# Kernel tuning notes

Measured on AMD Instinct MI355X. Metric: run time of the kernel, lower is better.

## Reference

```python
import jax, jax.numpy as jnp
import numpy as np

B, S, K = 128, 196, 512   # batch, encoder seq, keys_hidden_size
T_CAP = 16                # caption length (out_seq_len = 15)
V, E, H = 32000, 512, 512 # vocab, embedding, hidden


def setup_inputs() -> dict:
    key = jax.random.key(0)
    ks = jax.random.split(key, 16)
    sc = lambda fan_in: 1.0 / np.sqrt(fan_in)
    return {
        "features": jax.random.normal(ks[0], (B, S, K), jnp.float32),
        "captions": jax.random.randint(ks[1], (B, T_CAP), 0, V),
        "emb": jax.random.normal(ks[2], (V, E), jnp.float32) * 0.02,
        "fc1_w": jax.random.normal(ks[3], (H, E), jnp.float32) * sc(E),
        "fc1_b": jnp.zeros((H,), jnp.float32),
        "att_wq": jax.random.normal(ks[4], (H, H), jnp.float32) * sc(H),
        "att_wk": jax.random.normal(ks[5], (H, K), jnp.float32) * sc(K),
        "att_v": jax.random.normal(ks[6], (H,), jnp.float32) * sc(H),
        "fc0_w": jax.random.normal(ks[7], (H, K), jnp.float32) * sc(K),
        "fc0_b": jnp.zeros((H,), jnp.float32),
        "gru_wih": jax.random.normal(ks[8], (3 * H, 2 * H), jnp.float32) * sc(2 * H),
        "gru_whh": jax.random.normal(ks[9], (3 * H, H), jnp.float32) * sc(H),
        "gru_bih": jnp.zeros((3 * H,), jnp.float32),
        "gru_bhh": jnp.zeros((3 * H,), jnp.float32),
        "fc2_w": jax.random.normal(ks[10], (V, H), jnp.float32) * sc(H),
        "fc2_b": jnp.zeros((V,), jnp.float32),
    }


def reference(features, captions, emb, fc1_w, fc1_b, att_wq, att_wk, att_v,
              fc0_w, fc0_b, gru_wih, gru_whh, gru_bih, gru_bhh, fc2_w, fc2_b):
    # embed captions and project: (B, T_CAP, H)
    x = emb[captions] @ fc1_w.T + fc1_b
    # precompute key projection for Bahdanau attention: (B, S, H)
    keys_proj = features @ att_wk.T

    def step(h, x_t):
        # Bahdanau additive attention
        q = h @ att_wq.T                                   # (B, H)
        scores = jnp.tanh(q[:, None, :] + keys_proj) @ att_v  # (B, S)
        w = jax.nn.softmax(scores, axis=1)
        context = jnp.einsum('bs,bsk->bk', w, features)    # (B, K)
        context = context @ fc0_w.T + fc0_b                # fc_0 -> (B, H)
        rnn_in = jnp.concatenate([x_t, context], axis=-1)  # (B, 2H)
        # GRU cell, torch gate order (r, z, n)
        gi = rnn_in @ gru_wih.T + gru_bih
        gh = h @ gru_whh.T + gru_bhh
        ir, iz, inn = jnp.split(gi, 3, axis=-1)
        hr, hz, hn = jnp.split(gh, 3, axis=-1)
        r = jax.nn.sigmoid(ir + hr)
        z = jax.nn.sigmoid(iz + hz)
        n = jnp.tanh(inn + r * hn)
        h_new = (1.0 - z) * n + z * h
        out = h_new @ fc2_w.T + fc2_b                      # fc_2 -> (B, V)
        return h_new, out

    out_seq_len = captions.shape[1] - 1
    xs = jnp.swapaxes(x[:, :out_seq_len], 0, 1)            # (T, B, H)
    h0 = jnp.zeros((features.shape[0], fc0_b.shape[0]), features.dtype)
    _, outs = jax.lax.scan(step, h0, xs)                   # (T, B, V)
    return jnp.swapaxes(outs, 0, 1)                        # (B, T, V)
```

## Files before the change

### kernel.cpp

```cpp
#include <hip/hip_runtime.h>

typedef _Float16 half_t;
typedef float    floatx4 __attribute__((ext_vector_type(4)));
typedef _Float16 halfx8  __attribute__((ext_vector_type(8)));
typedef _Float16 halfx2  __attribute__((ext_vector_type(2)));

__device__ __forceinline__ float tanh_f(float x) {
  float e = __expf(2.0f * x);
  return 1.0f - 2.0f / (e + 1.0f);
}
__device__ __forceinline__ float sigmoid_f(float x) {
  return 1.0f / (1.0f + __expf(-x));
}

__device__ __forceinline__ void gl16(const void* g, void* s) {
  __builtin_amdgcn_global_load_lds((__attribute__((address_space(1))) unsigned int*)g,
                                   (__attribute__((address_space(3))) unsigned int*)s,
                                   16, 0, 0);
}

__device__ __forceinline__ int xcd_swz(int bid, int nwg) {
  int q = nwg >> 3, r = nwg & 7, x = bid & 7, p = bid >> 3;
  return (x < r ? x * (q + 1) : r * (q + 1) + (x - r) * q) + p;
}

__device__ __forceinline__ void cvt4(const float* __restrict__ src,
                                     half_t* __restrict__ dst, int blk) {
  int i = (blk * 256 + threadIdx.x) * 4;
  float4 v = *(const float4*)(src + i);
  halfx2 a; a[0] = (half_t)v.x; a[1] = (half_t)v.y;
  halfx2 b; b[0] = (half_t)v.z; b[1] = (half_t)v.w;
  *(halfx2*)(dst + i) = a;
  *(halfx2*)(dst + i + 2) = b;
}

__global__ __launch_bounds__(256) void k_prep(const float* __restrict__ fc2_w, half_t* __restrict__ fc2w_h,
                                              const float* __restrict__ features, half_t* __restrict__ featf,
                                              const float* __restrict__ fc1_w, half_t* __restrict__ fc1w_h,
                                              const float* __restrict__ att_wk, const float* __restrict__ fc0_w,
                                              half_t* __restrict__ wkfc0,
                                              const float* __restrict__ gru_whh, const float* __restrict__ att_wq,
                                              half_t* __restrict__ bcat2,
                                              const float* __restrict__ gru_wih, half_t* __restrict__ wihx,
                                              half_t* __restrict__ wihc,
                                              const float* __restrict__ emb, const int* __restrict__ cap,
                                              half_t* __restrict__ embg,
                                              const float* __restrict__ fc0_b, float* __restrict__ biasc,
                                              float4* __restrict__ zbase) {
  const int bb = blockIdx.x, tid = threadIdx.x;
  if (bb < 16000) {
    cvt4(fc2_w, fc2w_h, bb);
  } else if (bb < 28544) {
    cvt4(features, featf, bb - 16000);
  } else if (bb < 28800) {
    cvt4(fc1_w, fc1w_h, bb - 28544);
  } else if (bb < 29056) {
    cvt4(att_wk, wkfc0, bb - 28800);
  } else if (bb < 29312) {
    cvt4(fc0_w, wkfc0 + (size_t)512 * 512, bb - 29056);
  } else if (bb < 30080) {
    cvt4(gru_whh, bcat2, bb - 29312);
  } else if (bb < 30336) {
    cvt4(att_wq, bcat2 + (size_t)1536 * 512, bb - 30080);
  } else if (bb < 31872) {
    int row = bb - 30336, j = tid * 2;
    float2 a = *(const float2*)(gru_wih + (size_t)row * 1024 + j);
    float2 b = *(const float2*)(gru_wih + (size_t)row * 1024 + 512 + j);
    halfx2 ax; ax[0] = (half_t)a.x; ax[1] = (half_t)a.y;
    halfx2 bx; bx[0] = (half_t)b.x; bx[1] = (half_t)b.y;
    *(halfx2*)(wihx + (size_t)row * 512 + j) = ax;
    *(halfx2*)(wihc + (size_t)row * 512 + j) = bx;
  } else if (bb < 33792) {
    int row = bb - 31872;
    int b = row / 15, t = row - b * 15;
    int c = cap[b * 16 + t];
    const float* s = emb + (size_t)c * 512;
    int e = tid * 2;
    float2 v = *(const float2*)(s + e);
    halfx2 o; o[0] = (half_t)v.x; o[1] = (half_t)v.y;
    *(halfx2*)(embg + (size_t)row * 512 + e) = o;
  } else if (bb < 33796) {
    int i = (bb - 33792) * 256 + tid;
    biasc[i] = (i < 512) ? 0.f : fc0_b[i - 512];
  } else {
    zbase[(size_t)(bb - 33796) * 256 + tid] = make_float4(0.f, 0.f, 0.f, 0.f);
  }
}

__device__ __forceinline__ void gemm128_mfma(const half_t* __restrict__ Ap,
                                             const half_t* __restrict__ Bp,
                                             const int Kd,
                                             const int m0, const int n0,
                                             char* smem, floatx4 (&acc)[4][4]) {
  constexpr int ABYTES = 128 * 32 * 2;
  constexpr int BBYTES = 128 * 32 * 2;

  const int l = threadIdx.x & 63;
  const int w = threadIdx.x >> 6;

  const half_t* gA = Ap + (size_t)(m0 + w * 32 + (l >> 2)) * Kd + (l & 3) * 8;
  const half_t* gB = Bp + (size_t)(n0 + w * 32 + (l >> 2)) * Kd + (l & 3) * 8;

  const int fr = l & 15;
  const int kq = (l >> 4) * 8;
  const int mh = (w & 1) * 64;
  const int nh = (w >> 1) * 64;

#pragma unroll
  for (int i = 0; i < 4; ++i)
#pragma unroll
    for (int j = 0; j < 4; ++j) { floatx4 z = {0.f, 0.f, 0.f, 0.f}; acc[i][j] = z; }

  const int NT = Kd >> 5;

  auto stage = [&](int tt) {
    const int k0 = tt * 32;
    char* aD = smem + (tt & 1) * ABYTES;
    char* bD = smem + 2 * ABYTES + (tt & 1) * BBYTES;
    const half_t* g = gA + k0;
    gl16(g, aD + (w * 32) * 64);
    gl16(g + (size_t)16 * Kd, aD + (w * 32 + 16) * 64);
    const half_t* g2 = gB + k0;
    gl16(g2, bD + (w * 32) * 64);
    gl16(g2 + (size_t)16 * Kd, bD + (w * 32 + 16) * 64);
  };

  stage(0);

  for (int t = 0; t < NT; ++t) {
    __syncthreads();
    if (t + 1 < NT) stage(t + 1);
    const char* aB = smem + (t & 1) * ABYTES;
    const char* bB = smem + 2 * ABYTES + (t & 1) * BBYTES;
    halfx8 af[4], bf[4];
#pragma unroll
    for (int i = 0; i < 4; ++i) {
      af[i] = *(const halfx8*)((const half_t*)aB + (size_t)(mh + i * 16 + fr) * 32 + kq);
      bf[i] = *(const halfx8*)((const half_t*)bB + (size_t)(nh + i * 16 + fr) * 32 + kq);
    }
#pragma unroll
    for (int i = 0; i < 4; ++i)
#pragma unroll
      for (int j = 0; j < 4; ++j)
        acc[i][j] = __builtin_amdgcn_mfma_f32_16x16x32_f16(af[i], bf[j], acc[i][j], 0, 0, 0);
  }
}

template <bool OUT_F16>
__device__ __forceinline__ void gemm128_body(const half_t* __restrict__ Ap,
                                             const half_t* __restrict__ Bp,
                                             const float* __restrict__ bias,
                                             void* __restrict__ Cp,
                                             const int Kd, const int ldc,
                                             const int m0, const int n0,
                                             char* smem) {
  const int l = threadIdx.x & 63;
  const int w = threadIdx.x >> 6;
  const int mh = (w & 1) * 64;
  const int nh = (w >> 1) * 64;
  floatx4 acc[4][4];
  gemm128_mfma(Ap, Bp, Kd, m0, n0, smem, acc);

#pragma unroll
  for (int j = 0; j < 4; ++j) {
    const int n = n0 + nh + j * 16 + (l & 15);
    const float bv = bias ? bias[n] : 0.0f;
#pragma unroll
    for (int i = 0; i < 4; ++i) {
      const int mb = m0 + mh + i * 16 + (l >> 4) * 4;
#pragma unroll
      for (int r = 0; r < 4; ++r) {
        const float v = acc[i][j][r] + bv;
        const size_t ci = (size_t)(mb + r) * ldc + n;
        if constexpr (OUT_F16) ((half_t*)Cp)[ci] = (half_t)v;
        else                   ((float*)Cp)[ci] = v;
      }
    }
  }
}

template <bool OUT_F16>
__global__ __launch_bounds__(256) void k_gemm_lds(const half_t* __restrict__ Ap,
                                                  const half_t* __restrict__ Bp,
                                                  const float* __restrict__ bias,
                                                  void* __restrict__ Cp,
                                                  int Kd, int ldc) {
  __shared__ __align__(16) char smem[32768];
  gemm128_body<OUT_F16>(Ap, Bp, bias, Cp, Kd, ldc,
                        blockIdx.y * 128, blockIdx.x * 128, smem);
}

__global__ __launch_bounds__(256) void k_kpfp(const half_t* __restrict__ featf,
                                              const half_t* __restrict__ wkfc0,
                                              const float* __restrict__ biasc,
                                              half_t* __restrict__ kpfp) {
  __shared__ __align__(16) char smem[32768];
  const int w = (blockIdx.x & 7) * 196 + (blockIdx.x >> 3);
  const int n0 = (w & 7) * 128;
  const int m0 = (w >> 3) * 128;
  gemm128_body<true>(featf, wkfc0, biasc, kpfp, 512, 1024, m0, n0, smem);
}

__global__ __launch_bounds__(256) void k_fc2_final(const half_t* __restrict__ hall,
                                                   const half_t* __restrict__ fc2w,
                                                   const float* __restrict__ fc2b,
                                                   float* __restrict__ outp) {
  __shared__ __align__(16) char smem[64 * 132 * 4];
  const int wk = xcd_swz(blockIdx.x, 3750);
  const int m0 = (wk % 15) * 128;
  const int n0 = (wk / 15) * 128;

  const int tid = threadIdx.x;
  const int l = tid & 63;
  const int w = tid >> 6;
  const int nh = (w >> 1) * 64;

  floatx4 acc[4][4];
  gemm128_mfma(hall, fc2w, 512, m0, n0, smem, acc);

  const float4 bv4 = *(const float4*)(fc2b + n0 + (tid & 31) * 4);
  float* sf = (float*)smem;

#pragma unroll
  for (int h = 0; h < 2; ++h) {
    __syncthreads();
    if ((w & 1) == h) {
#pragma unroll
      for (int i = 0; i < 4; ++i)
#pragma unroll
        for (int j = 0; j < 4; ++j)
#pragma unroll
          for (int r = 0; r < 4; ++r)
            sf[(i * 16 + (l >> 4) * 4 + r) * 132 + nh + j * 16 + (l & 15)] = acc[i][j][r];
    }
    __syncthreads();
#pragma unroll
    for (int it = 0; it < 8; ++it) {
      const int row = it * 8 + (tid >> 5);
      float4 v = *(const float4*)&sf[row * 132 + (tid & 31) * 4];
      v.x += bv4.x; v.y += bv4.y; v.z += bv4.z; v.w += bv4.w;
      *(float4*)(outp + (size_t)(m0 + h * 64 + row) * 32000 + n0 + (tid & 31) * 4) = v;
    }
  }
}

__global__ __launch_bounds__(256) void k_scores(const half_t* __restrict__ kpfp,
                                                const float* __restrict__ ghq,
                                                const float* __restrict__ attv,
                                                float* __restrict__ scores) {
  int w = blockIdx.x * 4 + (threadIdx.x >> 6);
  int l = threadIdx.x & 63;
  int b = w / 196;
  halfx8 kv = *(const halfx8*)(kpfp + (size_t)w * 1024 + l * 8);
  const float* qr = ghq + (size_t)b * 2048 + 1536 + l * 8;
  float4 q0 = *(const float4*)qr;
  float4 q1 = *(const float4*)(qr + 4);
  float4 a0 = *(const float4*)(attv + l * 8);
  float4 a1 = *(const float4*)(attv + l * 8 + 4);
  float acc = a0.x * tanh_f(q0.x + (float)kv[0]);
  acc += a0.y * tanh_f(q0.y + (float)kv[1]);
  acc += a0.z * tanh_f(q0.z + (float)kv[2]);
  acc += a0.w * tanh_f(q0.w + (float)kv[3]);
  acc += a1.x * tanh_f(q1.x + (float)kv[4]);
  acc += a1.y * tanh_f(q1.y + (float)kv[5]);
  acc += a1.z * tanh_f(q1.z + (float)kv[6]);
  acc += a1.w * tanh_f(q1.w + (float)kv[7]);
#pragma unroll
  for (int off = 32; off > 0; off >>= 1) acc += __shfl_xor(acc, off, 64);
  if (l == 0) scores[w] = acc;
}

__global__ __launch_bounds__(256) void k_ctx(const float* __restrict__ scores,
                                             const half_t* __restrict__ kpfp,
                                             half_t* __restrict__ ctxo) {
  const int b = blockIdx.x, kt = blockIdx.y * 128, t = threadIdx.x;
  __shared__ float sw[196], red[256];
  float sc = (t < 196) ? scores[b * 196 + t] : -1e30f;
  red[t] = sc; __syncthreads();
  for (int o = 128; o > 0; o >>= 1) { if (t < o) red[t] = fmaxf(red[t], red[t + o]); __syncthreads(); }
  float mx = red[0]; __syncthreads();
  float e = (t < 196) ? __expf(sc - mx) : 0.f;
  red[t] = e; __syncthreads();
  for (int o = 128; o > 0; o >>= 1) { if (t < o) red[t] += red[t + o]; __syncthreads(); }
  float inv = 1.0f / red[0];
  if (t < 196) sw[t] = e * inv;
  __syncthreads();
  const int kk = t & 127, half = t >> 7, s0 = half * 98;
  const half_t* fp = kpfp + (size_t)(b * 196 + s0) * 1024 + 512 + kt + kk;
  float acc = 0.f;
#pragma unroll 7
  for (int i = 0; i < 98; ++i) acc += sw[s0 + i] * (float)fp[(size_t)i * 1024];
  red[t] = acc; __syncthreads();
  if (t < 128) ctxo[(size_t)b * 512 + kt + t] = (half_t)(red[t] + red[t + 128]);
}

__global__ __launch_bounds__(256) void k_gates(const float* __restrict__ gix,
                                               const float* __restrict__ gic,
                                               const float* __restrict__ ghq,
                                               const float* __restrict__ bih,
                                               const float* __restrict__ bhh,
                                               float* __restrict__ hbuf,
                                               half_t* __restrict__ hh,
                                               half_t* __restrict__ hall, int step) {
  int idx = blockIdx.x * 256 + threadIdx.x;
  int b = idx >> 9, n = idx & 511;
  const float* gx = gix + (size_t)(b * 15 + step) * 1536;
  const float* gc = gic + (size_t)b * 1536;
  const float* gh = ghq + (size_t)b * 2048;
  float ir  = gx[n]        + gc[n]        + bih[n];
  float iz  = gx[n + 512]  + gc[n + 512]  + bih[n + 512];
  float in_ = gx[n + 1024] + gc[n + 1024] + bih[n + 1024];
  float hr  = gh[n]        + bhh[n];
  float hz  = gh[n + 512]  + bhh[n + 512];
  float hn  = gh[n + 1024] + bhh[n + 1024];
  float r = sigmoid_f(ir + hr);
  float z = sigmoid_f(iz + hz);
  float nn = tanh_f(in_ + r * hn);
  float hv = (1.0f - z) * nn + z * hbuf[idx];
  hbuf[idx] = hv;
  half_t h16 = (half_t)hv;
  hh[idx] = h16;
  hall[(size_t)(b * 15 + step) * 512 + n] = h16;
}

extern "C" void kernel_launch(void* const* d_in, const int* in_sizes, int n_in,
                              void* d_out, int out_size, void* d_ws, size_t ws_size,
                              hipStream_t stream) {
  (void)in_sizes; (void)n_in; (void)out_size; (void)ws_size;
  const float* features = (const float*)d_in[0];
  const int*   captions = (const int*)d_in[1];
  const float* emb      = (const float*)d_in[2];
  const float* fc1_w    = (const float*)d_in[3];
  const float* fc1_b    = (const float*)d_in[4];
  const float* att_wq   = (const float*)d_in[5];
  const float* att_wk   = (const float*)d_in[6];
  const float* att_v    = (const float*)d_in[7];
  const float* fc0_w    = (const float*)d_in[8];
  const float* fc0_b    = (const float*)d_in[9];
  const float* gru_wih  = (const float*)d_in[10];
  const float* gru_whh  = (const float*)d_in[11];
  const float* gru_bih  = (const float*)d_in[12];
  const float* gru_bhh  = (const float*)d_in[13];
  const float* fc2_w    = (const float*)d_in[14];
  const float* fc2_b    = (const float*)d_in[15];
  float* out = (float*)d_out;

  char* p = (char*)d_ws;
  half_t* kpfp   = (half_t*)p; p += (size_t)25088 * 1024 * 2;
  half_t* fc2w_h = (half_t*)p; p += (size_t)32000 * 512 * 2;
  float*  gix    = (float*)p;  p += (size_t)1920 * 1536 * 4;
  half_t* wihx_h = (half_t*)p; p += (size_t)1536 * 512 * 2;
  half_t* wihc_h = (half_t*)p; p += (size_t)1536 * 512 * 2;
  half_t* bcat2  = (half_t*)p; p += (size_t)2048 * 512 * 2;
  half_t* wkfc0  = (half_t*)p; p += (size_t)1024 * 512 * 2;
  half_t* fc1w_h = (half_t*)p; p += (size_t)512 * 512 * 2;
  half_t* embg_h = (half_t*)p; p += (size_t)1920 * 512 * 2;
  half_t* xproj_h= (half_t*)p; p += (size_t)1920 * 512 * 2;
  float*  biasc  = (float*)p;  p += (size_t)1024 * 4;
  float*  ghq    = (float*)p;  p += (size_t)128 * 2048 * 4;
  float*  hbuf   = (float*)p;  p += (size_t)128 * 512 * 4;
  int*    bar    = (int*)p;    p += 16;
  float*  scores = (float*)p;  p += (size_t)128 * 196 * 4;
  float*  gic    = (float*)p;  p += (size_t)128 * 1536 * 4;
  half_t* ctxo   = (half_t*)p; p += (size_t)128 * 512 * 2;
  half_t* h_h    = (half_t*)p; p += (size_t)128 * 512 * 2;
  half_t* featf  = (half_t*)p; p += (size_t)25088 * 512 * 2;
  half_t* hall   = (half_t*)p; p += (size_t)1920 * 512 * 2;
  (void)bar;

  k_prep<<<dim3(34117), 256, 0, stream>>>(fc2_w, fc2w_h, features, featf,
                                          fc1_w, fc1w_h, att_wk, fc0_w, wkfc0,
                                          gru_whh, att_wq, bcat2,
                                          gru_wih, wihx_h, wihc_h,
                                          emb, captions, embg_h,
                                          fc0_b, biasc, (float4*)ghq);
  k_gemm_lds<true><<<dim3(4, 15), 256, 0, stream>>>(embg_h, fc1w_h, fc1_b, xproj_h, 512, 512);
  k_kpfp<<<dim3(1568), 256, 0, stream>>>(featf, wkfc0, biasc, kpfp);
  k_gemm_lds<false><<<dim3(12, 15), 256, 0, stream>>>(xproj_h, wihx_h, nullptr, gix, 512, 1536);

  for (int t = 0; t < 15; ++t) {
    k_scores<<<dim3(6272), 256, 0, stream>>>(kpfp, ghq, att_v, scores);
    k_ctx<<<dim3(128, 4), 256, 0, stream>>>(scores, kpfp, ctxo);
    k_gemm_lds<false><<<dim3(12, 1), 256, 0, stream>>>(ctxo, wihc_h, nullptr, gic, 512, 1536);
    k_gates<<<dim3(256), 256, 0, stream>>>(gix, gic, ghq, gru_bih, gru_bhh, hbuf, h_h, hall, t);
    k_gemm_lds<false><<<dim3(16, 1), 256, 0, stream>>>(h_h, bcat2, nullptr, ghq, 512, 2048);
  }
  k_fc2_final<<<dim3(3750), 256, 0, stream>>>(hall, fc2w_h, fc2_b, out);
}
```

Measured before the change: 1.201 ms.

## Fuse GRU gate update into hidden-state GEMM with ping-pong state buffers

Merges the per-step GRU gate kernel and the h·[Whh;Wq] GEMM into one 16-block kernel. Each block recomputes the full 128x512 gate update and writes the whole fp16 h_h itself, so it can start its GEMM tile after a block-level barrier instead of waiting on a separate launch. The ghq and hbuf buffers are double-buffered so blocks can read the previous step's values while others write the new ones. This removes one launch per timestep, but every block now redundantly loads all gate inputs (several MB per block per step) and re-runs the gate maths, which may cost more time than the launch it saves.

```diff
diff --git a/kernel.cpp b/kernel.cpp
--- a/kernel.cpp
+++ b/kernel.cpp
@@ -3,6 +3,7 @@
 typedef _Float16 half_t;
 typedef float    floatx4 __attribute__((ext_vector_type(4)));
 typedef _Float16 halfx8  __attribute__((ext_vector_type(8)));
+typedef _Float16 halfx4  __attribute__((ext_vector_type(4)));
 typedef _Float16 halfx2  __attribute__((ext_vector_type(2)));
 
 __device__ __forceinline__ float tanh_f(float x) {
@@ -294,33 +295,74 @@
   if (t < 128) ctxo[(size_t)b * 512 + kt + t] = (half_t)(red[t] + red[t + 128]);
 }
 
-__global__ __launch_bounds__(256) void k_gates(const float* __restrict__ gix,
-                                               const float* __restrict__ gic,
-                                               const float* __restrict__ ghq,
-                                               const float* __restrict__ bih,
-                                               const float* __restrict__ bhh,
-                                               float* __restrict__ hbuf,
-                                               half_t* __restrict__ hh,
-                                               half_t* __restrict__ hall, int step) {
-  int idx = blockIdx.x * 256 + threadIdx.x;
-  int b = idx >> 9, n = idx & 511;
-  const float* gx = gix + (size_t)(b * 15 + step) * 1536;
-  const float* gc = gic + (size_t)b * 1536;
-  const float* gh = ghq + (size_t)b * 2048;
-  float ir  = gx[n]        + gc[n]        + bih[n];
-  float iz  = gx[n + 512]  + gc[n + 512]  + bih[n + 512];
-  float in_ = gx[n + 1024] + gc[n + 1024] + bih[n + 1024];
-  float hr  = gh[n]        + bhh[n];
-  float hz  = gh[n + 512]  + bhh[n + 512];
-  float hn  = gh[n + 1024] + bhh[n + 1024];
-  float r = sigmoid_f(ir + hr);
-  float z = sigmoid_f(iz + hz);
-  float nn = tanh_f(in_ + r * hn);
-  float hv = (1.0f - z) * nn + z * hbuf[idx];
-  hbuf[idx] = hv;
-  half_t h16 = (half_t)hv;
-  hh[idx] = h16;
-  hall[(size_t)(b * 15 + step) * 512 + n] = h16;
+__global__ __launch_bounds__(256, 1) void k_hstep(const float* __restrict__ gix,
+                                                  const float* __restrict__ gic,
+                                                  const float* __restrict__ ghq_in,
+                                                  const float* __restrict__ bih,
+                                                  const float* __restrict__ bhh,
+                                                  const float* __restrict__ hbuf_in,
+                                                  float* __restrict__ hbuf_out,
+                                                  half_t* __restrict__ hall,
+                                                  half_t* __restrict__ h_h,
+                                                  const half_t* __restrict__ bcat2,
+                                                  float* __restrict__ ghq_out,
+                                                  int step) {
+  __shared__ __align__(16) char smem[32768];
+  const int tid = threadIdx.x, blk = blockIdx.x;
+
+#pragma unroll 4
+  for (int k = 0; k < 64; ++k) {
+    const int g = k * 256 + tid;
+    const int b = g >> 7, n = (g & 127) * 4;
+    const float* gx = gix + (size_t)(b * 15 + step) * 1536 + n;
+    const float* gc = gic + (size_t)b * 1536 + n;
+    const float* gh = ghq_in + (size_t)b * 2048 + n;
+    float4 x0 = *(const float4*)gx;
+    float4 x1 = *(const float4*)(gx + 512);
+    float4 x2 = *(const float4*)(gx + 1024);
+    float4 c0 = *(const float4*)gc;
+    float4 c1 = *(const float4*)(gc + 512);
+    float4 c2 = *(const float4*)(gc + 1024);
+    float4 g0 = *(const float4*)gh;
+    float4 g1 = *(const float4*)(gh + 512);
+    float4 g2 = *(const float4*)(gh + 1024);
+    float4 i0 = *(const float4*)(bih + n);
+    float4 i1 = *(const float4*)(bih + 512 + n);
+    float4 i2 = *(const float4*)(bih + 1024 + n);
+    float4 d0 = *(const float4*)(bhh + n);
+    float4 d1 = *(const float4*)(bhh + 512 + n);
+    float4 d2 = *(const float4*)(bhh + 1024 + n);
+    float4 hp = *(const float4*)(hbuf_in + (size_t)b * 512 + n);
+    const float* px0 = (const float*)&x0; const float* px1 = (const float*)&x1;
+    const float* px2 = (const float*)&x2;
+    const float* pc0 = (const float*)&c0; const float* pc1 = (const float*)&c1;
+    const float* pc2 = (const float*)&c2;
+    const float* pg0 = (const float*)&g0; const float* pg1 = (const float*)&g1;
+    const float* pg2 = (const float*)&g2;
+    const float* pi0 = (const float*)&i0; const float* pi1 = (const float*)&i1;
+    const float* pi2 = (const float*)&i2;
+    const float* pd0 = (const float*)&d0; const float* pd1 = (const float*)&d1;
+    const float* pd2 = (const float*)&d2;
+    const float* php = (const float*)&hp;
+    float hv[4];
+    halfx4 h4;
+#pragma unroll
+    for (int u = 0; u < 4; ++u) {
+      float r = sigmoid_f(px0[u] + pc0[u] + pi0[u] + pg0[u] + pd0[u]);
+      float z = sigmoid_f(px1[u] + pc1[u] + pi1[u] + pg1[u] + pd1[u]);
+      float nn = tanh_f(px2[u] + pc2[u] + pi2[u] + r * (pg2[u] + pd2[u]));
+      hv[u] = (1.0f - z) * nn + z * php[u];
+      h4[u] = (half_t)hv[u];
+    }
+    *(halfx4*)(h_h + (size_t)b * 512 + n) = h4;
+    if ((g >> 10) == blk) {
+      *(float4*)(hbuf_out + (size_t)b * 512 + n) = make_float4(hv[0], hv[1], hv[2], hv[3]);
+      *(halfx4*)(hall + (size_t)(b * 15 + step) * 512 + n) = h4;
+    }
+  }
+  __syncthreads();
+
+  gemm128_body<false>(h_h, bcat2, nullptr, ghq_out, 512, 2048, 0, blk * 128, smem);
 }
 
 extern "C" void kernel_launch(void* const* d_in, const int* in_sizes, int n_in,
@@ -357,33 +399,37 @@
   half_t* embg_h = (half_t*)p; p += (size_t)1920 * 512 * 2;
   half_t* xproj_h= (half_t*)p; p += (size_t)1920 * 512 * 2;
   float*  biasc  = (float*)p;  p += (size_t)1024 * 4;
-  float*  ghq    = (float*)p;  p += (size_t)128 * 2048 * 4;
-  float*  hbuf   = (float*)p;  p += (size_t)128 * 512 * 4;
-  int*    bar    = (int*)p;    p += 16;
+  float*  ghq0   = (float*)p;  p += (size_t)128 * 2048 * 4;
+  float*  hbuf0  = (float*)p;  p += (size_t)128 * 512 * 4;
+  float*  ghq1   = (float*)p;  p += (size_t)128 * 2048 * 4;
+  float*  hbuf1  = (float*)p;  p += (size_t)128 * 512 * 4;
   float*  scores = (float*)p;  p += (size_t)128 * 196 * 4;
   float*  gic    = (float*)p;  p += (size_t)128 * 1536 * 4;
   half_t* ctxo   = (half_t*)p; p += (size_t)128 * 512 * 2;
   half_t* h_h    = (half_t*)p; p += (size_t)128 * 512 * 2;
   half_t* featf  = (half_t*)p; p += (size_t)25088 * 512 * 2;
   half_t* hall   = (half_t*)p; p += (size_t)1920 * 512 * 2;
-  (void)bar;
-
-  k_prep<<<dim3(34117), 256, 0, stream>>>(fc2_w, fc2w_h, features, featf,
+
+  k_prep<<<dim3(34116), 256, 0, stream>>>(fc2_w, fc2w_h, features, featf,
                                           fc1_w, fc1w_h, att_wk, fc0_w, wkfc0,
                                           gru_whh, att_wq, bcat2,
                                           gru_wih, wihx_h, wihc_h,
                                           emb, captions, embg_h,
-                                          fc0_b, biasc, (float4*)ghq);
+                                          fc0_b, biasc, (float4*)ghq0);
   k_gemm_lds<true><<<dim3(4, 15), 256, 0, stream>>>(embg_h, fc1w_h, fc1_b, xproj_h, 512, 512);
   k_kpfp<<<dim3(1568), 256, 0, stream>>>(featf, wkfc0, biasc, kpfp);
   k_gemm_lds<false><<<dim3(12, 15), 256, 0, stream>>>(xproj_h, wihx_h, nullptr, gix, 512, 1536);
 
   for (int t = 0; t < 15; ++t) {
-    k_scores<<<dim3(6272), 256, 0, stream>>>(kpfp, ghq, att_v, scores);
+    const float* gin  = (t & 1) ? ghq1 : ghq0;
+    float*       gout = (t & 1) ? ghq0 : ghq1;
+    const float* hin  = (t & 1) ? hbuf1 : hbuf0;
+    float*       hout = (t & 1) ? hbuf0 : hbuf1;
+    k_scores<<<dim3(6272), 256, 0, stream>>>(kpfp, gin, att_v, scores);
     k_ctx<<<dim3(128, 4), 256, 0, stream>>>(scores, kpfp, ctxo);
     k_gemm_lds<false><<<dim3(12, 1), 256, 0, stream>>>(ctxo, wihc_h, nullptr, gic, 512, 1536);
-    k_gates<<<dim3(256), 256, 0, stream>>>(gix, gic, ghq, gru_bih, gru_bhh, hbuf, h_h, hall, t);
-    k_gemm_lds<false><<<dim3(16, 1), 256, 0, stream>>>(h_h, bcat2, nullptr, ghq, 512, 2048);
+    k_hstep<<<dim3(16), 256, 0, stream>>>(gix, gic, gin, gru_bih, gru_bhh,
+                                          hin, hout, hall, h_h, bcat2, gout, t);
   }
   k_fc2_final<<<dim3(3750), 256, 0, stream>>>(hall, fc2w_h, fc2_b, out);
 }
```

New measurement: 2.031 ms. +69.2%, slower.
